# Kernel optimization log

Measured on AMD Instinct MI355X. Metric: run time of the kernel, lower is better.

The kernel has to match this reference:

```python
import jax, jax.numpy as jnp
import numpy as np

N, E = 50000, 400000
EMB, IN, HID, HEADS = 128, 128, 128, 3
RRELU_SLOPE = (1.0 / 8.0 + 1.0 / 3.0) / 2.0  # torch.rrelu eval-mode slope


def _gat_conv(h_in, src, dst, W, a_src, a_dst, b, concat):
    """PyG-style GATConv. h_in: [N, F_in]; src/dst: [E'] (self-loops included)."""
    n = h_in.shape[0]
    h = (h_in @ W).reshape(n, HEADS, -1)            # [N, H, C]
    e_src = jnp.sum(h * a_src, axis=-1)             # [N, H]
    e_dst = jnp.sum(h * a_dst, axis=-1)             # [N, H]
    e = jax.nn.leaky_relu(e_src[src] + e_dst[dst], 0.2)  # [E', H]
    # softmax over incoming edges of each target node
    m = jax.ops.segment_max(e, dst, num_segments=n)
    ex = jnp.exp(e - m[dst])
    denom = jax.ops.segment_sum(ex, dst, num_segments=n)
    alpha = ex / denom[dst]                          # [E', H]
    out = jax.ops.segment_sum(h[src] * alpha[:, :, None], dst, num_segments=n)  # [N,H,C]
    out = out.reshape(n, -1) if concat else out.mean(axis=1)
    return out + b


def _rrelu(x):
    return jnp.where(x >= 0, x, x * RRELU_SLOPE)


def setup_inputs() -> dict:
    key = jax.random.key(0)
    ks = jax.random.split(key, 16)
    d_in = IN + EMB

    def glorot(k, shape):
        fan = sum(shape)
        return jax.random.normal(k, shape, jnp.float32) * np.sqrt(2.0 / fan)

    return {
        "z": jax.random.normal(ks[0], (N, EMB), jnp.float32),
        "x": jax.random.normal(ks[1], (N, IN), jnp.float32),
        "ei": jax.random.randint(ks[2], (2, E), 0, N, jnp.int32),
        "W1": glorot(ks[3], (d_in, HEADS * HID)),
        "a1_src": glorot(ks[4], (HEADS, HID)),
        "a1_dst": glorot(ks[5], (HEADS, HID)),
        "b1": jnp.zeros((HID,), jnp.float32),                 # concat=False -> size C
        "W2": glorot(ks[6], (HID, HEADS * HID)),
        "a2_src": glorot(ks[7], (HEADS, HID)),
        "a2_dst": glorot(ks[8], (HEADS, HID)),
        "b2": jnp.zeros((HEADS * HID,), jnp.float32),         # concat=True -> size H*C
        "W_lin": glorot(ks[9], (HEADS * HID, 1)),
        "b_lin": jnp.zeros((1,), jnp.float32),
    }


def reference(z, x, ei, W1, a1_src, a1_dst, b1, W2, a2_src, a2_dst, b2, W_lin, b_lin):
    n = x.shape[0]
    loops = jnp.arange(n, dtype=ei.dtype)
    src = jnp.concatenate([ei[0], loops])  # PyG add_self_loops=True
    dst = jnp.concatenate([ei[1], loops])
    h = jnp.concatenate([z, x], axis=1)
    h = _rrelu(_gat_conv(h, src, dst, W1, a1_src, a1_dst, b1, concat=False))
    h = _rrelu(_gat_conv(h, src, dst, W2, a2_src, a2_dst, b2, concat=True))
    return jax.nn.sigmoid(h @ W_lin + b_lin)
```

## Files before the change

kernel.cpp:

```cpp
#include <hip/hip_runtime.h>
#include <stdint.h>

#define HEADS 3
#define HID 128
#define FDIM (HEADS * HID)

typedef __attribute__((ext_vector_type(8))) short bf16x8;
typedef __attribute__((ext_vector_type(4))) float f32x4;

__device__ __forceinline__ float lrelu(float x) { return x >= 0.f ? x : 0.2f * x; }
__device__ __forceinline__ float rrelu(float x) {
    const float SLOPE = (1.0f / 8.0f + 1.0f / 3.0f) * 0.5f;
    return x >= 0.f ? x : SLOPE * x;
}
__device__ __forceinline__ unsigned short f2bf(float f) {
    union { float f; unsigned u; } c; c.f = f;
    unsigned r = c.u + 0x7FFF + ((c.u >> 16) & 1);
    return (unsigned short)(r >> 16);
}
__device__ __forceinline__ float bflo(unsigned u) {
    union { unsigned u; float f; } c; c.u = u << 16; return c.f;
}
__device__ __forceinline__ float bfhi(unsigned u) {
    union { unsigned u; float f; } c; c.u = u & 0xffff0000u; return c.f;
}

__device__ __forceinline__ void gload_lds16(const void* g, void* l) {
    __builtin_amdgcn_global_load_lds(
        (const __attribute__((address_space(1))) void*)g,
        (__attribute__((address_space(3))) void*)l, 16, 0, 0);
}


__global__ void k_hist(const int* __restrict__ dst, int E, int* __restrict__ cnt) {
    for (int i = blockIdx.x * blockDim.x + threadIdx.x; i < E; i += gridDim.x * blockDim.x)
        atomicAdd(&cnt[dst[i]], 1);
}

#define SC_T 256
#define SC_E 8
#define SC_CHUNK (SC_T * SC_E)

__global__ __launch_bounds__(SC_T) void k_scan1(const int* __restrict__ cnt,
                                                int* __restrict__ exc,
                                                int* __restrict__ bsum, int n) {
    __shared__ int sm[SC_T];
    int b = blockIdx.x, t = threadIdx.x;
    int base = b * SC_CHUNK + t * SC_E;
    int v[SC_E];
    int s = 0;
#pragma unroll
    for (int i = 0; i < SC_E; i++) {
        int idx = base + i;
        v[i] = (idx < n) ? cnt[idx] : 0;
        s += v[i];
    }
    sm[t] = s;
    __syncthreads();
    for (int off = 1; off < SC_T; off <<= 1) {
        int x = (t >= off) ? sm[t - off] : 0;
        __syncthreads();
        sm[t] += x;
        __syncthreads();
    }
    int run = sm[t] - s;
    if (t == SC_T - 1) bsum[b] = sm[t];
#pragma unroll
    for (int i = 0; i < SC_E; i++) {
        int idx = base + i;
        if (idx < n) exc[idx] = run;
        run += v[i];
    }
}

__global__ __launch_bounds__(256) void k_scan2(const int* __restrict__ bsum,
                                               int* __restrict__ bpre, int nb) {
    __shared__ int sm[256];
    int t = threadIdx.x;
    int v = (t < nb) ? bsum[t] : 0;
    sm[t] = v;
    __syncthreads();
    for (int off = 1; off < 256; off <<= 1) {
        int x = (t >= off) ? sm[t - off] : 0;
        __syncthreads();
        sm[t] += x;
        __syncthreads();
    }
    if (t < nb) bpre[t + 1] = sm[t];
    if (t == 0) bpre[0] = 0;
}

__global__ void k_scan3(int* __restrict__ offs, const int* __restrict__ bpre,
                        int* __restrict__ cursor, int n, int nb) {
    int i = blockIdx.x * blockDim.x + threadIdx.x;
    if (i < n) {
        int o = offs[i] + bpre[i / SC_CHUNK];
        offs[i] = o;
        cursor[i] = o;
    }
    if (i == 0) offs[n] = bpre[nb];
}

__global__ void k_scatter(const int* __restrict__ src, const int* __restrict__ dst, int E,
                          int* __restrict__ cursor, int* __restrict__ ssrc,
                          int* __restrict__ sdst) {
    for (int i = blockIdx.x * blockDim.x + threadIdx.x; i < E; i += gridDim.x * blockDim.x) {
        int d = dst[i];
        int p = atomicAdd(&cursor[d], 1);
        ssrc[p] = src[i];
        sdst[p] = d;
    }
}


__global__ void k_cvt_concat(const float* __restrict__ z, const float* __restrict__ x,
                             unsigned short* __restrict__ A, int Nn, int Mpad) {
    int total = Mpad * 64;
    for (int i = blockIdx.x * blockDim.x + threadIdx.x; i < total;
         i += gridDim.x * blockDim.x) {
        int row = i >> 6;
        int c4 = (i & 63) * 4;
        float4 v = make_float4(0.f, 0.f, 0.f, 0.f);
        if (row < Nn) {
            const float* sp = (c4 < 128) ? (z + (size_t)row * 128 + c4)
                                         : (x + (size_t)row * 128 + (c4 - 128));
            v = *(const float4*)sp;
        }
        unsigned short o[4] = {f2bf(v.x), f2bf(v.y), f2bf(v.z), f2bf(v.w)};
        *(uint2*)&A[(size_t)row * 256 + c4] = *(uint2*)o;
    }
}

__global__ void k_cvt_wt(const float* __restrict__ W, unsigned short* __restrict__ WT,
                         int K, int Ncols) {
    int n = blockIdx.x;
    for (int k = threadIdx.x; k < K; k += blockDim.x)
        WT[(size_t)n * K + k] = f2bf(W[(size_t)k * Ncols + n]);
}


__global__ __launch_bounds__(256) void k_gemm_bf16(
    const unsigned short* __restrict__ A,
    const unsigned short* __restrict__ BT,
    unsigned short* __restrict__ C,
    int K, int Ncols,
    const float* __restrict__ asrc, const float* __restrict__ adst,
    float* __restrict__ es, float* __restrict__ ed, int Nnodes) {
    __shared__ __align__(16) unsigned short As[128 * 32];
    __shared__ __align__(16) unsigned short Bs[128 * 32];
    __shared__ float esP[128][2], edP[128][2];
    int tid = threadIdx.x;
    int w = tid >> 6, lane = tid & 63;
    int row0 = blockIdx.x * 128;
    int col0 = blockIdx.y * 128;
    int wr = w >> 1, wc = w & 1;

    f32x4 acc[4][4] = {};
    int frow = lane & 15;
    int fk = (lane >> 4) * 8;

    for (int k0 = 0; k0 < K; k0 += 32) {
#pragma unroll
        for (int i = 0; i < 2; i++) {
            int c = (i * 4 + w) * 64 + lane;
            gload_lds16(A + (size_t)(row0 + (c >> 2)) * K + k0 + (c & 3) * 8,
                        (char*)As + (i * 4 + w) * 1024);
        }
#pragma unroll
        for (int i = 0; i < 2; i++) {
            int c = (i * 4 + w) * 64 + lane;
            gload_lds16(BT + (size_t)(col0 + (c >> 2)) * K + k0 + (c & 3) * 8,
                        (char*)Bs + (i * 4 + w) * 1024);
        }
        asm volatile("s_waitcnt vmcnt(0)" ::: "memory");
        __syncthreads();

        bf16x8 af[4], bfr[4];
#pragma unroll
        for (int m = 0; m < 4; m++)
            af[m] = *(const bf16x8*)&As[(wr * 64 + m * 16 + frow) * 32 + fk];
#pragma unroll
        for (int n = 0; n < 4; n++)
            bfr[n] = *(const bf16x8*)&Bs[(wc * 64 + n * 16 + frow) * 32 + fk];
#pragma unroll
        for (int m = 0; m < 4; m++)
#pragma unroll
            for (int n = 0; n < 4; n++)
                acc[m][n] = __builtin_amdgcn_mfma_f32_16x16x32_bf16(af[m], bfr[n], acc[m][n], 0, 0, 0);
        __syncthreads();
    }

    int ccol = lane & 15, crow = (lane >> 4) * 4;

#pragma unroll
    for (int m = 0; m < 4; m++)
#pragma unroll
        for (int n = 0; n < 4; n++)
#pragma unroll
            for (int j = 0; j < 4; j++) {
                int r = row0 + wr * 64 + m * 16 + crow + j;
                int cc = col0 + wc * 64 + n * 16 + ccol;
                C[(size_t)r * Ncols + cc] = f2bf(acc[m][n][j]);
            }

    int head = blockIdx.y;
    float as4[4], ad4[4];
#pragma unroll
    for (int n = 0; n < 4; n++) {
        int col_sub = wc * 64 + n * 16 + ccol;
        as4[n] = asrc[head * HID + col_sub];
        ad4[n] = adst[head * HID + col_sub];
    }
#pragma unroll
    for (int m = 0; m < 4; m++)
#pragma unroll
        for (int j = 0; j < 4; j++) {
            float ps = 0.f, pd = 0.f;
#pragma unroll
            for (int n = 0; n < 4; n++) {
                float v = acc[m][n][j];
                ps = fmaf(v, as4[n], ps);
                pd = fmaf(v, ad4[n], pd);
            }
#pragma unroll
            for (int off = 1; off < 16; off <<= 1) {
                ps += __shfl_xor(ps, off);
                pd += __shfl_xor(pd, off);
            }
            if (ccol == 0) {
                int row_sub = wr * 64 + m * 16 + crow + j;
                esP[row_sub][wc] = ps;
                edP[row_sub][wc] = pd;
            }
        }
    __syncthreads();
    if (tid < 128) {
        int r = row0 + tid;
        if (r < Nnodes) {
            es[(size_t)r * 3 + head] = esP[tid][0] + esP[tid][1];
            ed[(size_t)r * 3 + head] = edP[tid][0] + edP[tid][1];
        }
    }
}


__global__ void k_edge_w(const int* __restrict__ ssrc, const int* __restrict__ sdst,
                         const float* __restrict__ es, const float* __restrict__ ed,
                         float4* __restrict__ w4, int E) {
    for (int j = blockIdx.x * blockDim.x + threadIdx.x; j < E; j += gridDim.x * blockDim.x) {
        int s = ssrc[j], d = sdst[j];
        float w0 = __expf(lrelu(es[s * 3 + 0] + ed[d * 3 + 0]));
        float w1 = __expf(lrelu(es[s * 3 + 1] + ed[d * 3 + 1]));
        float w2 = __expf(lrelu(es[s * 3 + 2] + ed[d * 3 + 2]));
        w4[j] = make_float4(w0, w1, w2, 0.f);
    }
}

__global__ void k_den(const float* __restrict__ es, const float* __restrict__ ed,
                      const int* __restrict__ offs, const float4* __restrict__ w4,
                      float4* __restrict__ wself, float4* __restrict__ invden, int Nn) {
    for (int n = blockIdx.x * blockDim.x + threadIdx.x; n < Nn; n += gridDim.x * blockDim.x) {
        float s0 = __expf(lrelu(es[n * 3 + 0] + ed[n * 3 + 0]));
        float s1 = __expf(lrelu(es[n * 3 + 1] + ed[n * 3 + 1]));
        float s2 = __expf(lrelu(es[n * 3 + 2] + ed[n * 3 + 2]));
        float d0 = s0, d1 = s1, d2 = s2;
        int j0 = offs[n], j1 = offs[n + 1];
        int j = j0;
        for (; j + 4 <= j1; j += 4) {
            float4 a = w4[j], b = w4[j + 1], c = w4[j + 2], d = w4[j + 3];
            d0 += a.x + b.x + c.x + d.x;
            d1 += a.y + b.y + c.y + d.y;
            d2 += a.z + b.z + c.z + d.z;
        }
        for (; j < j1; j++) {
            float4 w = w4[j];
            d0 += w.x; d1 += w.y; d2 += w.z;
        }
        wself[n] = make_float4(s0, s1, s2, 0.f);
        invden[n] = make_float4(1.f / d0, 1.f / d1, 1.f / d2, 0.f);
    }
}


#define AGG_BODY(acc_update)                                                      \
    int j = j0;                                                                   \
    for (; j + 8 <= j1; j += 8) {                                                 \
        int s[8]; float wv[8]; unsigned uu[8];                                    \
        _Pragma("unroll") for (int e = 0; e < 8; e++) s[e] = ssrc[j + e];         \
        _Pragma("unroll") for (int e = 0; e < 8; e++)                             \
            wv[e] = w4f[(size_t)(j + e) * 4 + h];                                 \
        _Pragma("unroll") for (int e = 0; e < 8; e++)                             \
            uu[e] = Hu[(size_t)s[e] * 192 + cidx];                                \
        _Pragma("unroll") for (int e = 0; e < 8; e++) { acc_update(wv[e], uu[e]) }\
    }                                                                             \
    for (; j + 4 <= j1; j += 4) {                                                 \
        int s[4]; float wv[4]; unsigned uu[4];                                    \
        _Pragma("unroll") for (int e = 0; e < 4; e++) s[e] = ssrc[j + e];         \
        _Pragma("unroll") for (int e = 0; e < 4; e++)                             \
            wv[e] = w4f[(size_t)(j + e) * 4 + h];                                 \
        _Pragma("unroll") for (int e = 0; e < 4; e++)                             \
            uu[e] = Hu[(size_t)s[e] * 192 + cidx];                                \
        _Pragma("unroll") for (int e = 0; e < 4; e++) { acc_update(wv[e], uu[e]) }\
    }                                                                             \
    for (; j < j1; j++) {                                                         \
        int s = ssrc[j];                                                          \
        float w = w4f[(size_t)j * 4 + h];                                         \
        unsigned u1 = Hu[(size_t)s * 192 + cidx];                                 \
        { acc_update(w, u1) }                                                     \
    }

#define ACC_UPD(wv, uv) a0 = fmaf(wv, bflo(uv), a0); a1 = fmaf(wv, bfhi(uv), a1);

__global__ __launch_bounds__(192) void k_gat_mean(const unsigned short* __restrict__ H,
                                                  const float* __restrict__ w4f,
                                                  const float* __restrict__ wselff,
                                                  const float* __restrict__ invdenf,
                                                  const int* __restrict__ offs,
                                                  const int* __restrict__ ssrc,
                                                  const float* __restrict__ b,
                                                  unsigned short* __restrict__ out, int Nn) {
    int n = blockIdx.x;
    int t = threadIdx.x;
    int h = t >> 6, q = t & 63;
    int cidx = (h * HID + 2 * q) >> 1;
    const unsigned* Hu = (const unsigned*)H;
    unsigned u = Hu[(size_t)n * 192 + cidx];
    float wsh = wselff[n * 4 + h];
    float a0 = wsh * bflo(u), a1 = wsh * bfhi(u);
    int j0 = offs[n], j1 = offs[n + 1];
    AGG_BODY(ACC_UPD)
    float iv = invdenf[n * 4 + h];
    a0 *= iv; a1 *= iv;
    __shared__ float sm[3][128];
    sm[h][2 * q] = a0;
    sm[h][2 * q + 1] = a1;
    __syncthreads();
    if (t < 64) {
        int c0 = 2 * t;
        float m0 = (sm[0][c0] + sm[1][c0] + sm[2][c0]) * (1.f / 3.f) + b[c0];
        float m1 = (sm[0][c0 + 1] + sm[1][c0 + 1] + sm[2][c0 + 1]) * (1.f / 3.f) + b[c0 + 1];
        unsigned short o[2] = {f2bf(rrelu(m0)), f2bf(rrelu(m1))};
        *(unsigned*)&out[(size_t)n * HID + c0] = *(unsigned*)o;
    }
}


__global__ __launch_bounds__(192) void k_gat_cat_final(const unsigned short* __restrict__ H,
                                                       const float* __restrict__ w4f,
                                                       const float* __restrict__ wselff,
                                                       const float* __restrict__ invdenf,
                                                       const int* __restrict__ offs,
                                                       const int* __restrict__ ssrc,
                                                       const float* __restrict__ b,
                                                       const float* __restrict__ Wl,
                                                       const float* __restrict__ bl,
                                                       float* __restrict__ out, int Nn) {
    int n = blockIdx.x;
    int t = threadIdx.x;
    int h = t >> 6, q = t & 63;
    int col = h * HID + 2 * q;
    int cidx = col >> 1;
    const unsigned* Hu = (const unsigned*)H;
    unsigned u = Hu[(size_t)n * 192 + cidx];
    float wsh = wselff[n * 4 + h];
    float a0 = wsh * bflo(u), a1 = wsh * bfhi(u);
    int j0 = offs[n], j1 = offs[n + 1];
    AGG_BODY(ACC_UPD)
    float iv = invdenf[n * 4 + h];
    float r0 = rrelu(a0 * iv + b[col]);
    float r1 = rrelu(a1 * iv + b[col + 1]);
    float p = r0 * Wl[col] + r1 * Wl[col + 1];
#pragma unroll
    for (int off = 32; off > 0; off >>= 1) p += __shfl_down(p, off);
    __shared__ float red[3];
    if (q == 0) red[h] = p;
    __syncthreads();
    if (t == 0) out[n] = 1.f / (1.f + __expf(-(red[0] + red[1] + red[2] + bl[0])));
}


extern "C" void kernel_launch(void* const* d_in, const int* in_sizes, int n_in,
                              void* d_out, int out_size, void* d_ws, size_t ws_size,
                              hipStream_t stream) {
    const float* z   = (const float*)d_in[0];
    const float* x   = (const float*)d_in[1];
    const int*   ei  = (const int*)d_in[2];
    const float* W1  = (const float*)d_in[3];
    const float* a1s = (const float*)d_in[4];
    const float* a1d = (const float*)d_in[5];
    const float* b1  = (const float*)d_in[6];
    const float* W2  = (const float*)d_in[7];
    const float* a2s = (const float*)d_in[8];
    const float* a2d = (const float*)d_in[9];
    const float* b2  = (const float*)d_in[10];
    const float* Wl  = (const float*)d_in[11];
    const float* bl  = (const float*)d_in[12];
    float* outp = (float*)d_out;

    int Nn = in_sizes[0] / 128;
    int E  = in_sizes[2] / 2;
    int Mpad = (Nn + 127) & ~127;
    int nb = (Nn + SC_CHUNK - 1) / SC_CHUNK;

    char* p = (char*)d_ws;
    auto carve = [&](size_t bytes) -> char* {
        char* r = p;
        p += (bytes + 255) & ~(size_t)255;
        return r;
    };
    int*            offs   = (int*)carve((size_t)(Nn + 1) * 4);
    int*            cursor = (int*)carve((size_t)Nn * 4);
    int*            ssrc   = (int*)carve((size_t)E * 4);
    int*            sdst   = (int*)carve((size_t)E * 4);
    int*            bsum   = (int*)carve((size_t)(nb + 1) * 4);
    int*            bpre   = (int*)carve((size_t)(nb + 1) * 4);
    float*          e1s    = (float*)carve((size_t)Nn * 3 * 4);
    float*          e1d    = (float*)carve((size_t)Nn * 3 * 4);
    float4*         w4     = (float4*)carve((size_t)E * 16);
    float4*         wself  = (float4*)carve((size_t)Nn * 16);
    float4*         invden = (float4*)carve((size_t)Nn * 16);
    unsigned short* Abf    = (unsigned short*)carve((size_t)Mpad * 256 * 2);
    unsigned short* W1T    = (unsigned short*)carve((size_t)FDIM * 256 * 2);
    unsigned short* W2T    = (unsigned short*)carve((size_t)FDIM * 128 * 2);
    unsigned short* Hbf    = (unsigned short*)carve((size_t)Mpad * FDIM * 2);
    unsigned short* H2in   = (unsigned short*)carve((size_t)Mpad * 128 * 2);

    const int* srcI = ei;
    const int* dstI = ei + E;

    hipMemsetAsync(cursor, 0, (size_t)Nn * 4, stream);
    k_hist<<<256, 256, 0, stream>>>(dstI, E, cursor);
    k_scan1<<<nb, SC_T, 0, stream>>>(cursor, offs, bsum, Nn);
    k_scan2<<<1, 256, 0, stream>>>(bsum, bpre, nb);
    k_scan3<<<(Nn + 255) / 256, 256, 0, stream>>>(offs, bpre, cursor, Nn, nb);
    k_scatter<<<256, 256, 0, stream>>>(srcI, dstI, E, cursor, ssrc, sdst);

    k_cvt_concat<<<2048, 256, 0, stream>>>(z, x, Abf, Nn, Mpad);
    k_cvt_wt<<<FDIM, 256, 0, stream>>>(W1, W1T, 256, FDIM);
    k_cvt_wt<<<FDIM, 128, 0, stream>>>(W2, W2T, 128, FDIM);
    hipMemsetAsync(H2in + (size_t)Nn * 128, 0, (size_t)(Mpad - Nn) * 128 * 2, stream);

    dim3 gg(Mpad / 128, FDIM / 128);

    k_gemm_bf16<<<gg, 256, 0, stream>>>(Abf, W1T, Hbf, 256, FDIM, a1s, a1d, e1s, e1d, Nn);
    k_edge_w<<<1024, 256, 0, stream>>>(ssrc, sdst, e1s, e1d, w4, E);
    k_den<<<(Nn + 255) / 256, 256, 0, stream>>>(e1s, e1d, offs, w4, wself, invden, Nn);
    k_gat_mean<<<Nn, 192, 0, stream>>>(Hbf, (const float*)w4, (const float*)wself,
                                       (const float*)invden, offs, ssrc, b1, H2in, Nn);

    k_gemm_bf16<<<gg, 256, 0, stream>>>(H2in, W2T, Hbf, 128, FDIM, a2s, a2d, e1s, e1d, Nn);
    k_edge_w<<<1024, 256, 0, stream>>>(ssrc, sdst, e1s, e1d, w4, E);
    k_den<<<(Nn + 255) / 256, 256, 0, stream>>>(e1s, e1d, offs, w4, wself, invden, Nn);
    k_gat_cat_final<<<Nn, 192, 0, stream>>>(Hbf, (const float*)w4, (const float*)wself,
                                            (const float*)invden, offs, ssrc, b2, Wl, bl,
                                            outp, Nn);
}
```

Before: 267.2 us.

## Aggregate one node per wavefront in grid-stride loop, all heads per lane

The two GAT aggregation kernels change from one 192-thread block per node to a persistent grid of 256-thread blocks where each 64-lane wavefront handles one node. Each lane covers all three heads, loading one float4 of edge weights and three row words per edge. This removes the shared-memory head reduction and the __syncthreads, and cuts the per-edge index and weight loads by sharing them across heads. The cost is a longer serial edge loop per wavefront, only 4-way unroll instead of 8, and more registers per lane.

```diff
diff --git a/kernel.cpp b/kernel.cpp
--- a/kernel.cpp
+++ b/kernel.cpp
@@ -282,100 +282,95 @@
 }
 
 
-#define AGG_BODY(acc_update)                                                      \
-    int j = j0;                                                                   \
-    for (; j + 8 <= j1; j += 8) {                                                 \
-        int s[8]; float wv[8]; unsigned uu[8];                                    \
-        _Pragma("unroll") for (int e = 0; e < 8; e++) s[e] = ssrc[j + e];         \
-        _Pragma("unroll") for (int e = 0; e < 8; e++)                             \
-            wv[e] = w4f[(size_t)(j + e) * 4 + h];                                 \
-        _Pragma("unroll") for (int e = 0; e < 8; e++)                             \
-            uu[e] = Hu[(size_t)s[e] * 192 + cidx];                                \
-        _Pragma("unroll") for (int e = 0; e < 8; e++) { acc_update(wv[e], uu[e]) }\
-    }                                                                             \
-    for (; j + 4 <= j1; j += 4) {                                                 \
-        int s[4]; float wv[4]; unsigned uu[4];                                    \
-        _Pragma("unroll") for (int e = 0; e < 4; e++) s[e] = ssrc[j + e];         \
-        _Pragma("unroll") for (int e = 0; e < 4; e++)                             \
-            wv[e] = w4f[(size_t)(j + e) * 4 + h];                                 \
-        _Pragma("unroll") for (int e = 0; e < 4; e++)                             \
-            uu[e] = Hu[(size_t)s[e] * 192 + cidx];                                \
-        _Pragma("unroll") for (int e = 0; e < 4; e++) { acc_update(wv[e], uu[e]) }\
-    }                                                                             \
-    for (; j < j1; j++) {                                                         \
-        int s = ssrc[j];                                                          \
-        float w = w4f[(size_t)j * 4 + h];                                         \
-        unsigned u1 = Hu[(size_t)s * 192 + cidx];                                 \
-        { acc_update(w, u1) }                                                     \
-    }
-
-#define ACC_UPD(wv, uv) a0 = fmaf(wv, bflo(uv), a0); a1 = fmaf(wv, bfhi(uv), a1);
-
-__global__ __launch_bounds__(192) void k_gat_mean(const unsigned short* __restrict__ H,
-                                                  const float* __restrict__ w4f,
-                                                  const float* __restrict__ wselff,
-                                                  const float* __restrict__ invdenf,
+#define EDGE_UNROLL4(body)                                                       \
+    int j = j0;                                                                  \
+    for (; j + 4 <= j1; j += 4) {                                                \
+        int si[4]; float4 wv[4]; unsigned uu[4][3];                              \
+        _Pragma("unroll") for (int e = 0; e < 4; e++) si[e] = ssrc[j + e];       \
+        _Pragma("unroll") for (int e = 0; e < 4; e++) wv[e] = w4[j + e];         \
+        _Pragma("unroll") for (int e = 0; e < 4; e++) {                          \
+            const unsigned* rp = Hu + (size_t)si[e] * 192 + L;                   \
+            uu[e][0] = rp[0]; uu[e][1] = rp[64]; uu[e][2] = rp[128];             \
+        }                                                                        \
+        _Pragma("unroll") for (int e = 0; e < 4; e++) { body(wv[e], uu[e]) }     \
+    }                                                                            \
+    for (; j < j1; j++) {                                                        \
+        int s1_ = ssrc[j]; float4 w_ = w4[j];                                    \
+        const unsigned* rp = Hu + (size_t)s1_ * 192 + L;                         \
+        unsigned u_[3] = {rp[0], rp[64], rp[128]};                               \
+        { body(w_, u_) }                                                         \
+    }
+
+#define ACC3(wv, uv)                                                             \
+    a0[0] = fmaf(wv.x, bflo(uv[0]), a0[0]); a1[0] = fmaf(wv.x, bfhi(uv[0]), a1[0]); \
+    a0[1] = fmaf(wv.y, bflo(uv[1]), a0[1]); a1[1] = fmaf(wv.y, bfhi(uv[1]), a1[1]); \
+    a0[2] = fmaf(wv.z, bflo(uv[2]), a0[2]); a1[2] = fmaf(wv.z, bfhi(uv[2]), a1[2]);
+
+__global__ __launch_bounds__(256) void k_agg_mean(const unsigned* __restrict__ Hu,
+                                                  const float4* __restrict__ w4,
+                                                  const float4* __restrict__ wself,
+                                                  const float4* __restrict__ invden,
                                                   const int* __restrict__ offs,
                                                   const int* __restrict__ ssrc,
                                                   const float* __restrict__ b,
-                                                  unsigned short* __restrict__ out, int Nn) {
-    int n = blockIdx.x;
-    int t = threadIdx.x;
-    int h = t >> 6, q = t & 63;
-    int cidx = (h * HID + 2 * q) >> 1;
-    const unsigned* Hu = (const unsigned*)H;
-    unsigned u = Hu[(size_t)n * 192 + cidx];
-    float wsh = wselff[n * 4 + h];
-    float a0 = wsh * bflo(u), a1 = wsh * bfhi(u);
-    int j0 = offs[n], j1 = offs[n + 1];
-    AGG_BODY(ACC_UPD)
-    float iv = invdenf[n * 4 + h];
-    a0 *= iv; a1 *= iv;
-    __shared__ float sm[3][128];
-    sm[h][2 * q] = a0;
-    sm[h][2 * q + 1] = a1;
-    __syncthreads();
-    if (t < 64) {
-        int c0 = 2 * t;
-        float m0 = (sm[0][c0] + sm[1][c0] + sm[2][c0]) * (1.f / 3.f) + b[c0];
-        float m1 = (sm[0][c0 + 1] + sm[1][c0 + 1] + sm[2][c0 + 1]) * (1.f / 3.f) + b[c0 + 1];
+                                                  unsigned* __restrict__ out, int Nn) {
+    int L = threadIdx.x & 63;
+    int wstep = gridDim.x * 4;
+    for (int n = blockIdx.x * 4 + (threadIdx.x >> 6); n < Nn; n += wstep) {
+        float4 ws = wself[n];
+        const unsigned* rp = Hu + (size_t)n * 192 + L;
+        unsigned u0 = rp[0], u1 = rp[64], u2 = rp[128];
+        float a0[3] = {ws.x * bflo(u0), ws.y * bflo(u1), ws.z * bflo(u2)};
+        float a1[3] = {ws.x * bfhi(u0), ws.y * bfhi(u1), ws.z * bfhi(u2)};
+        int j0 = offs[n], j1 = offs[n + 1];
+        EDGE_UNROLL4(ACC3)
+        float4 iv = invden[n];
+        int c0 = 2 * L;
+        float2 bb = *(const float2*)&b[c0];
+        float m0 = (a0[0] * iv.x + a0[1] * iv.y + a0[2] * iv.z) * (1.f / 3.f) + bb.x;
+        float m1 = (a1[0] * iv.x + a1[1] * iv.y + a1[2] * iv.z) * (1.f / 3.f) + bb.y;
         unsigned short o[2] = {f2bf(rrelu(m0)), f2bf(rrelu(m1))};
-        *(unsigned*)&out[(size_t)n * HID + c0] = *(unsigned*)o;
-    }
-}
-
-
-__global__ __launch_bounds__(192) void k_gat_cat_final(const unsigned short* __restrict__ H,
-                                                       const float* __restrict__ w4f,
-                                                       const float* __restrict__ wselff,
-                                                       const float* __restrict__ invdenf,
+        out[(size_t)n * 64 + L] = *(unsigned*)o;
+    }
+}
+
+__global__ __launch_bounds__(256) void k_agg_cat_final(const unsigned* __restrict__ Hu,
+                                                       const float4* __restrict__ w4,
+                                                       const float4* __restrict__ wself,
+                                                       const float4* __restrict__ invden,
                                                        const int* __restrict__ offs,
                                                        const int* __restrict__ ssrc,
                                                        const float* __restrict__ b,
                                                        const float* __restrict__ Wl,
                                                        const float* __restrict__ bl,
                                                        float* __restrict__ out, int Nn) {
-    int n = blockIdx.x;
-    int t = threadIdx.x;
-    int h = t >> 6, q = t & 63;
-    int col = h * HID + 2 * q;
-    int cidx = col >> 1;
-    const unsigned* Hu = (const unsigned*)H;
-    unsigned u = Hu[(size_t)n * 192 + cidx];
-    float wsh = wselff[n * 4 + h];
-    float a0 = wsh * bflo(u), a1 = wsh * bfhi(u);
-    int j0 = offs[n], j1 = offs[n + 1];
-    AGG_BODY(ACC_UPD)
-    float iv = invdenf[n * 4 + h];
-    float r0 = rrelu(a0 * iv + b[col]);
-    float r1 = rrelu(a1 * iv + b[col + 1]);
-    float p = r0 * Wl[col] + r1 * Wl[col + 1];
-#pragma unroll
-    for (int off = 32; off > 0; off >>= 1) p += __shfl_down(p, off);
-    __shared__ float red[3];
-    if (q == 0) red[h] = p;
-    __syncthreads();
-    if (t == 0) out[n] = 1.f / (1.f + __expf(-(red[0] + red[1] + red[2] + bl[0])));
+    int L = threadIdx.x & 63;
+    int wstep = gridDim.x * 4;
+    for (int n = blockIdx.x * 4 + (threadIdx.x >> 6); n < Nn; n += wstep) {
+        float4 ws = wself[n];
+        const unsigned* rp = Hu + (size_t)n * 192 + L;
+        unsigned u0 = rp[0], u1 = rp[64], u2 = rp[128];
+        float a0[3] = {ws.x * bflo(u0), ws.y * bflo(u1), ws.z * bflo(u2)};
+        float a1[3] = {ws.x * bfhi(u0), ws.y * bfhi(u1), ws.z * bfhi(u2)};
+        int j0 = offs[n], j1 = offs[n + 1];
+        EDGE_UNROLL4(ACC3)
+        float4 iv = invden[n];
+        float ivv[3] = {iv.x, iv.y, iv.z};
+        float p = 0.f;
+#pragma unroll
+        for (int k = 0; k < 3; k++) {
+            int col = k * HID + 2 * L;
+            float2 bb = *(const float2*)&b[col];
+            float2 wl = *(const float2*)&Wl[col];
+            float r0 = rrelu(a0[k] * ivv[k] + bb.x);
+            float r1 = rrelu(a1[k] * ivv[k] + bb.y);
+            p = fmaf(r0, wl.x, p);
+            p = fmaf(r1, wl.y, p);
+        }
+#pragma unroll
+        for (int off = 32; off > 0; off >>= 1) p += __shfl_down(p, off);
+        if (L == 0) out[n] = 1.f / (1.f + __expf(-(p + bl[0])));
+    }
 }
 
 
@@ -445,13 +440,12 @@
     k_gemm_bf16<<<gg, 256, 0, stream>>>(Abf, W1T, Hbf, 256, FDIM, a1s, a1d, e1s, e1d, Nn);
     k_edge_w<<<1024, 256, 0, stream>>>(ssrc, sdst, e1s, e1d, w4, E);
     k_den<<<(Nn + 255) / 256, 256, 0, stream>>>(e1s, e1d, offs, w4, wself, invden, Nn);
-    k_gat_mean<<<Nn, 192, 0, stream>>>(Hbf, (const float*)w4, (const float*)wself,
-                                       (const float*)invden, offs, ssrc, b1, H2in, Nn);
+    k_agg_mean<<<2048, 256, 0, stream>>>((const unsigned*)Hbf, w4, wself, invden, offs,
+                                         ssrc, b1, (unsigned*)H2in, Nn);
 
     k_gemm_bf16<<<gg, 256, 0, stream>>>(H2in, W2T, Hbf, 128, FDIM, a2s, a2d, e1s, e1d, Nn);
     k_edge_w<<<1024, 256, 0, stream>>>(ssrc, sdst, e1s, e1d, w4, E);
     k_den<<<(Nn + 255) / 256, 256, 0, stream>>>(e1s, e1d, offs, w4, wself, invden, Nn);
-    k_gat_cat_final<<<Nn, 192, 0, stream>>>(Hbf, (const float*)w4, (const float*)wself,
-                                            (const float*)invden, offs, ssrc, b2, Wl, bl,
-                                            outp, Nn);
-}
+    k_agg_cat_final<<<2048, 256, 0, stream>>>((const unsigned*)Hbf, w4, wself, invden, offs,
+                                              ssrc, b2, Wl, bl, outp, Nn);
+}
```

Measured after the change: 266.7 us. No clear change (-0.2%).
